# Kernel optimization log

Hardware: AMD Instinct MI355X
Metric: run time of the kernel (lower is better)

The kernel has to match this reference:

```python
import jax, jax.numpy as jnp
import numpy as np

D_MODEL = 256
N_HEADS = 8
N_LEVELS = 4
N_POINTS = 4
DH = D_MODEL // N_HEADS
SHAPES = [(100, 150), (50, 75), (25, 38), (13, 19)]  # per-level (H, W)
BATCH = 2


def setup_inputs() -> dict:
    key = jax.random.key(0)
    ks = jax.random.split(key, 8)
    Lq = sum(h * w for h, w in SHAPES)  # 19947
    d = D_MODEL
    off_dim = N_HEADS * N_LEVELS * N_POINTS * 2
    aw_dim = N_HEADS * N_LEVELS * N_POINTS
    s = 1.0 / np.sqrt(d).astype(np.float32)
    lsi = np.concatenate([[0], np.cumsum([h * w for h, w in SHAPES])[:-1]])
    return {
        "query": jax.random.normal(ks[0], (BATCH, Lq, d), jnp.float32),
        "reference_points": jax.random.uniform(ks[1], (BATCH, Lq, N_LEVELS, 2), jnp.float32),
        "input_flatten": jax.random.normal(ks[2], (BATCH, Lq, d), jnp.float32),
        "input_spatial_shapes": jnp.array(SHAPES, dtype=jnp.int32),
        "input_level_start_index": jnp.array(lsi, dtype=jnp.int32),
        "W_samp": 0.01 * jax.random.normal(ks[3], (off_dim, d), jnp.float32),
        "b_samp": 0.1 * jax.random.normal(ks[4], (off_dim,), jnp.float32),
        "W_attn": s * jax.random.normal(ks[5], (aw_dim, d), jnp.float32),
        "b_attn": jnp.zeros((aw_dim,), jnp.float32),
        "W_val": s * jax.random.normal(ks[6], (d, d), jnp.float32),
        "b_val": jnp.zeros((d,), jnp.float32),
        "W_out": s * jax.random.normal(ks[7], (d, d), jnp.float32),
        "b_out": jnp.zeros((d,), jnp.float32),
    }


def _bilinear(v, grid, Hl, Wl):
    # v: [N, H, Hl*Wl, Dh] flattened level feature map per head
    # grid: [N, H, Q, P, 2] in [-1, 1]; align_corners=False, zero padding
    N, H, Q, P, _ = grid.shape
    Dh = v.shape[-1]
    x = (grid[..., 0] + 1.0) * 0.5 * Wl - 0.5
    y = (grid[..., 1] + 1.0) * 0.5 * Hl - 0.5
    x0 = jnp.floor(x)
    y0 = jnp.floor(y)
    lx = x - x0
    ly = y - y0
    x0i = x0.astype(jnp.int32)
    y0i = y0.astype(jnp.int32)

    def corner(xi, yi, w):
        valid = (xi >= 0) & (xi < Wl) & (yi >= 0) & (yi < Hl)
        idx = jnp.clip(yi, 0, Hl - 1) * Wl + jnp.clip(xi, 0, Wl - 1)
        g = jnp.take_along_axis(v, idx.reshape(N, H, Q * P, 1), axis=2)
        return g.reshape(N, H, Q, P, Dh) * (w * valid)[..., None]

    return (corner(x0i, y0i, (1 - lx) * (1 - ly))
            + corner(x0i + 1, y0i, lx * (1 - ly))
            + corner(x0i, y0i + 1, (1 - lx) * ly)
            + corner(x0i + 1, y0i + 1, lx * ly))


def _forward(query, ref, x, shapes, W_samp, b_samp, W_attn, b_attn, W_val, b_val, W_out, b_out):
    N, Lq, d = query.shape
    H, L, P, Dh = N_HEADS, N_LEVELS, N_POINTS, DH
    # value projection -> [N, H, S, Dh]
    value = (x @ W_val.T + b_val).reshape(N, -1, H, Dh).transpose(0, 2, 1, 3)
    off = (query @ W_samp.T + b_samp).reshape(N, Lq, H, L, P, 2)
    attw = jax.nn.softmax((query @ W_attn.T + b_attn).reshape(N, Lq, H, L * P), axis=-1)
    attw = attw.reshape(N, Lq, H, L, P).transpose(0, 2, 1, 3, 4)  # [N,H,Lq,L,P]
    # offset normalizer is (W, H) per level
    norm = jnp.array([[w, h] for h, w in shapes], dtype=query.dtype)  # [L, 2]
    loc = ref[:, :, None, :, None, :] + off / norm[None, None, None, :, None, :]
    grids = (2.0 * loc - 1.0).transpose(0, 2, 1, 3, 4, 5)  # [N,H,Lq,L,P,2]

    acc = jnp.zeros((N, Lq, H, Dh), query.dtype)
    start = 0
    for lvl, (Hl, Wl) in enumerate(shapes):
        v = value[:, :, start:start + Hl * Wl]  # [N,H,Hl*Wl,Dh]
        start += Hl * Wl
        samp = _bilinear(v, grids[:, :, :, lvl], Hl, Wl)  # [N,H,Lq,P,Dh]
        acc = acc + jnp.einsum('nhqpd,nhqp->nqhd', samp, attw[:, :, :, lvl])
    out = acc.reshape(N, Lq, H * Dh)
    return out @ W_out.T + b_out


def reference(query, reference_points, input_flatten, input_spatial_shapes,
              input_level_start_index, W_samp, b_samp, W_attn, b_attn,
              W_val, b_val, W_out, b_out):
    shapes = [(int(h), int(w)) for h, w in np.asarray(input_spatial_shapes)]
    return _forward(query, reference_points, input_flatten, shapes,
                    W_samp, b_samp, W_attn, b_attn, W_val, b_val, W_out, b_out)
```

## Files before the change

kernel.cpp:

```cpp
#include <hip/hip_runtime.h>
#include <hip/hip_bf16.h>

#define NB 2
#define LQ 19947
#define LV 19947
#define DM 256
#define NH 8
#define NL 4
#define NP 4
#define MROWS (NB*LQ)
#define MPAD  39936
#define QPB 2

__device__ __constant__ int c_lvlH[4] = {100, 50, 25, 13};
__device__ __constant__ int c_lvlW[4] = {150, 75, 38, 19};
__device__ __constant__ int c_lvlS[4] = {0, 15000, 18750, 19700};

typedef __attribute__((ext_vector_type(8))) short short8;
typedef __attribute__((ext_vector_type(4))) float f32x4;

__device__ __forceinline__ unsigned short f2bf(float f) {
  unsigned u = __float_as_uint(f);
  u += 0x7FFFu + ((u >> 16) & 1u);
  return (unsigned short)(u >> 16);
}
__device__ __forceinline__ float bfl(unsigned u) { return __uint_as_float(u << 16); }
__device__ __forceinline__ float bfh(unsigned u) { return __uint_as_float(u & 0xFFFF0000u); }

#define CB_X 9984
__global__ __launch_bounds__(256) void conv_all(
    const float* __restrict__ xin, const float* __restrict__ query,
    const float* __restrict__ Wv, const float* __restrict__ Wsamp,
    const float* __restrict__ Wattn, const float* __restrict__ Wout,
    const float* __restrict__ bsamp, const float* __restrict__ battn,
    unsigned short* __restrict__ xb, unsigned short* __restrict__ qb,
    unsigned short* __restrict__ wvb, unsigned short* __restrict__ wqb,
    unsigned short* __restrict__ wob, float* __restrict__ bsa)
{
  const int b = blockIdx.x, t = threadIdx.x;
  if (b == 2 * CB_X + 224) {
    bsa[t] = bsamp[t];
    if (t < 128) bsa[256 + t] = battn[t];
    return;
  }
  const float* src; unsigned short* dst; int base, ns;
  if (b < CB_X)            { src = xin;   dst = xb;          base = b * 1024;                ns = MROWS * 256; }
  else if (b < 2*CB_X)     { src = query; dst = qb;          base = (b - CB_X) * 1024;       ns = MROWS * 256; }
  else if (b < 2*CB_X+64)  { src = Wv;    dst = wvb;         base = (b - 2*CB_X) * 1024;     ns = 65536; }
  else if (b < 2*CB_X+128) { src = Wsamp; dst = wqb;         base = (b - 2*CB_X-64) * 1024;  ns = 65536; }
  else if (b < 2*CB_X+160) { src = Wattn; dst = wqb + 65536; base = (b - 2*CB_X-128) * 1024; ns = 32768; }
  else                     { src = Wout;  dst = wob;         base = (b - 2*CB_X-160) * 1024; ns = 65536; }
  const int i = base + t * 4;
  ushort4 o;
  if (i + 4 <= ns) {
    const float4 v = *(const float4*)(src + i);
    o.x = f2bf(v.x); o.y = f2bf(v.y); o.z = f2bf(v.z); o.w = f2bf(v.w);
  } else {
    float vs[4];
    #pragma unroll
    for (int j = 0; j < 4; ++j) vs[j] = (i + j < ns) ? src[i + j] : 0.f;
    o.x = f2bf(vs[0]); o.y = f2bf(vs[1]); o.z = f2bf(vs[2]); o.w = f2bf(vs[3]);
  }
  *(ushort4*)(dst + i) = o;
}

__global__ __launch_bounds__(256) void gemm_front(
    const unsigned short* __restrict__ xb, const unsigned short* __restrict__ qb,
    const unsigned short* __restrict__ wvb, const unsigned short* __restrict__ wqb,
    const float* __restrict__ b_val, const float* __restrict__ bsa,
    unsigned short* __restrict__ value, unsigned short* __restrict__ oc)
{
  const unsigned short* Ab; const unsigned short* Wb; const float* bias;
  unsigned short* Cp; int Nn, cb;
  if (blockIdx.y < 2) { Ab = xb; Wb = wvb; bias = b_val; Cp = value; Nn = 256; cb = blockIdx.y; }
  else                { Ab = qb; Wb = wqb; bias = bsa;   Cp = oc;    Nn = 384; cb = blockIdx.y - 2; }

  __shared__ alignas(16) short As[128 * 32];
  __shared__ alignas(16) short Bs[128 * 32];

  const int t = threadIdx.x;
  const int w = t >> 6, l = t & 63;
  const int wr = w >> 1, wc = w & 1;
  const size_t rowBase = (size_t)blockIdx.x * 128;
  const int colBase = cb * 128;

  const f32x4 z = {0.f, 0.f, 0.f, 0.f};
  f32x4 acc[4][4];
  #pragma unroll
  for (int i = 0; i < 4; ++i)
    #pragma unroll
    for (int j = 0; j < 4; ++j) acc[i][j] = z;

  const int srow = l >> 2;
  const int scol = (l & 3) * 8;

  for (int ks = 0; ks < 8; ++ks) {
    const int k0 = ks * 32;
    #pragma unroll
    for (int i = 0; i < 2; ++i) {
      const int ii = w * 2 + i;
      const unsigned short* gA = Ab + (rowBase + ii * 16 + srow) * 256 + k0 + scol;
      __builtin_amdgcn_global_load_lds(
          (const __attribute__((address_space(1))) void*)gA,
          (__attribute__((address_space(3))) void*)&As[ii * 512], 16, 0, 0);
      const unsigned short* gB = Wb + ((size_t)(colBase + ii * 16 + srow)) * 256 + k0 + scol;
      __builtin_amdgcn_global_load_lds(
          (const __attribute__((address_space(1))) void*)gB,
          (__attribute__((address_space(3))) void*)&Bs[ii * 512], 16, 0, 0);
    }
    __syncthreads();
    short8 af[4], bf[4];
    #pragma unroll
    for (int i = 0; i < 4; ++i) {
      af[i] = *(const short8*)&As[(wr * 64 + i * 16 + (l & 15)) * 32 + (l >> 4) * 8];
      bf[i] = *(const short8*)&Bs[(wc * 64 + i * 16 + (l & 15)) * 32 + (l >> 4) * 8];
    }
    #pragma unroll
    for (int i = 0; i < 4; ++i)
      #pragma unroll
      for (int j = 0; j < 4; ++j)
        acc[i][j] = __builtin_amdgcn_mfma_f32_16x16x32_bf16(bf[j], af[i], acc[i][j], 0, 0, 0);
    __syncthreads();
  }

  const int row0 = (int)rowBase + wr * 64 + (l & 15);
  const int col0 = colBase + wc * 64 + (l >> 4) * 4;
  #pragma unroll
  for (int j = 0; j < 4; ++j) {
    const float4 bj = *(const float4*)(bias + col0 + j * 16);
    #pragma unroll
    for (int i = 0; i < 4; ++i) {
      const int row = row0 + i * 16;
      uint2 st;
      st.x = (unsigned)f2bf(acc[i][j][0] + bj.x) | ((unsigned)f2bf(acc[i][j][1] + bj.y) << 16);
      st.y = (unsigned)f2bf(acc[i][j][2] + bj.z) | ((unsigned)f2bf(acc[i][j][3] + bj.w) << 16);
      *(uint2*)(Cp + (size_t)row * Nn + col0 + j * 16) = st;
    }
  }
}

__global__ __launch_bounds__(256) void gemm_out(
    const unsigned short* __restrict__ Ab, const unsigned short* __restrict__ Wb,
    const float* __restrict__ bias, float* __restrict__ Cp)
{
  __shared__ alignas(16) short As[128 * 32];
  __shared__ alignas(16) short Bs[128 * 32];

  const int t = threadIdx.x;
  const int w = t >> 6, l = t & 63;
  const int wr = w >> 1, wc = w & 1;
  const size_t rowBase = (size_t)blockIdx.x * 128;
  const int colBase = blockIdx.y * 128;

  const f32x4 z = {0.f, 0.f, 0.f, 0.f};
  f32x4 acc[4][4];
  #pragma unroll
  for (int i = 0; i < 4; ++i)
    #pragma unroll
    for (int j = 0; j < 4; ++j) acc[i][j] = z;

  const int srow = l >> 2;
  const int scol = (l & 3) * 8;

  for (int ks = 0; ks < 8; ++ks) {
    const int k0 = ks * 32;
    #pragma unroll
    for (int i = 0; i < 2; ++i) {
      const int ii = w * 2 + i;
      const unsigned short* gA = Ab + (rowBase + ii * 16 + srow) * 256 + k0 + scol;
      __builtin_amdgcn_global_load_lds(
          (const __attribute__((address_space(1))) void*)gA,
          (__attribute__((address_space(3))) void*)&As[ii * 512], 16, 0, 0);
      const unsigned short* gB = Wb + ((size_t)(colBase + ii * 16 + srow)) * 256 + k0 + scol;
      __builtin_amdgcn_global_load_lds(
          (const __attribute__((address_space(1))) void*)gB,
          (__attribute__((address_space(3))) void*)&Bs[ii * 512], 16, 0, 0);
    }
    __syncthreads();
    short8 af[4], bf[4];
    #pragma unroll
    for (int i = 0; i < 4; ++i) {
      af[i] = *(const short8*)&As[(wr * 64 + i * 16 + (l & 15)) * 32 + (l >> 4) * 8];
      bf[i] = *(const short8*)&Bs[(wc * 64 + i * 16 + (l & 15)) * 32 + (l >> 4) * 8];
    }
    #pragma unroll
    for (int i = 0; i < 4; ++i)
      #pragma unroll
      for (int j = 0; j < 4; ++j)
        acc[i][j] = __builtin_amdgcn_mfma_f32_16x16x32_bf16(bf[j], af[i], acc[i][j], 0, 0, 0);
    __syncthreads();
  }

  const int row0 = (int)rowBase + wr * 64 + (l & 15);
  const int col0 = colBase + wc * 64 + (l >> 4) * 4;
  #pragma unroll
  for (int j = 0; j < 4; ++j) {
    const float4 bj = *(const float4*)(bias + col0 + j * 16);
    #pragma unroll
    for (int i = 0; i < 4; ++i) {
      const int row = row0 + i * 16;
      if (row < MROWS) {
        *(float4*)(Cp + (size_t)row * 256 + col0 + j * 16) =
            make_float4(acc[i][j][0] + bj.x, acc[i][j][1] + bj.y,
                        acc[i][j][2] + bj.z, acc[i][j][3] + bj.w);
      }
    }
  }
}

__global__ __launch_bounds__(128) void msda_sample(
    const unsigned short* __restrict__ value,
    const float* __restrict__ refp,
    const unsigned short* __restrict__ oc,
    unsigned short* __restrict__ accb)
{
  __shared__ float s_aw[QPB][128];
  __shared__ float s_ref[QPB][8];
  __shared__ alignas(16) unsigned s_poff[QPB][NH][17][4];
  __shared__ alignas(16) float    s_pw[QPB][NH][17][4];

  const int t = threadIdx.x;
  const int bq0 = blockIdx.x * QPB;

  {
    const int q = t >> 6, i = t & 63;
    const int bq = bq0 + q;
    const unsigned pw = *(const unsigned*)(oc + (size_t)bq * 384 + 256 + i * 2);
    s_aw[q][i * 2 + 0] = bfl(pw);
    s_aw[q][i * 2 + 1] = bfh(pw);
    if (t < QPB * 8) {
      const int q2 = t >> 3, j = t & 7;
      s_ref[q2][j] = refp[(size_t)(bq0 + q2) * 8 + j];
    }
  }
  __syncthreads();

  if (t < QPB * NH) {
    const int q = t >> 3, h = t & 7;
    float* aw = &s_aw[q][h * 16];
    float m = aw[0];
    #pragma unroll
    for (int i = 1; i < 16; ++i) m = fmaxf(m, aw[i]);
    float e[16]; float s = 0.f;
    #pragma unroll
    for (int i = 0; i < 16; ++i) { e[i] = __expf(aw[i] - m); s += e[i]; }
    const float inv = 1.f / s;
    #pragma unroll
    for (int i = 0; i < 16; ++i) aw[i] = e[i] * inv;
  }
  __syncthreads();

  #pragma unroll
  for (int it = t; it < QPB * 128; it += 128) {
    const int q = it >> 7, rem = it & 127;
    const int h = rem >> 4, idx = rem & 15;
    const int l = idx >> 2;
    const int bq = bq0 + q;
    const unsigned po = *(const unsigned*)(oc + (size_t)bq * 384 + rem * 2);
    const int Hl = c_lvlH[l], Wl = c_lvlW[l], st = c_lvlS[l];
    const float x = s_ref[q][l * 2 + 0] * (float)Wl - 0.5f + bfl(po);
    const float y = s_ref[q][l * 2 + 1] * (float)Hl - 0.5f + bfh(po);
    const float aw = s_aw[q][rem];
    const float x0f = floorf(x), y0f = floorf(y);
    const float lx = x - x0f, ly = y - y0f;
    const int x0 = (int)x0f, y0 = (int)y0f;
    const float vx0 = (x0 >= 0 && x0 < Wl) ? 1.f : 0.f;
    const float vx1 = (x0 >= -1 && x0 < Wl - 1) ? 1.f : 0.f;
    const float vy0 = (y0 >= 0 && y0 < Hl) ? 1.f : 0.f;
    const float vy1 = (y0 >= -1 && y0 < Hl - 1) ? 1.f : 0.f;
    const int xc0 = min(max(x0, 0), Wl - 1);
    const int xc1 = min(max(x0 + 1, 0), Wl - 1);
    const int yc0 = min(max(y0, 0), Hl - 1);
    const int yc1 = min(max(y0 + 1, 0), Hl - 1);
    const int r0 = st + yc0 * Wl, r1 = st + yc1 * Wl;
    s_poff[q][h][idx][0] = (unsigned)(r0 + xc0) * 512u;
    s_poff[q][h][idx][1] = (unsigned)(r0 + xc1) * 512u;
    s_poff[q][h][idx][2] = (unsigned)(r1 + xc0) * 512u;
    s_poff[q][h][idx][3] = (unsigned)(r1 + xc1) * 512u;
    s_pw[q][h][idx][0] = (1.f - lx) * (1.f - ly) * aw * (vx0 * vy0);
    s_pw[q][h][idx][1] = lx * (1.f - ly) * aw * (vx1 * vy0);
    s_pw[q][h][idx][2] = (1.f - lx) * ly * aw * (vx0 * vy1);
    s_pw[q][h][idx][3] = lx * ly * aw * (vx1 * vy1);
  }
  __syncthreads();

  const int w = t >> 6;
  const int lane = t & 63;
  const int bq = bq0 + w;
  const int n = bq / LQ;
  const char* vbase = (const char*)value + (size_t)n * LV * 512;
  const int h = lane >> 3;
  const int laneoff = h * 64 + (lane & 7) * 8;

  float a0 = 0.f, a1 = 0.f, a2 = 0.f, a3 = 0.f;
  #pragma unroll
  for (int idx = 0; idx < 16; ++idx) {
    const uint4  of = *(const uint4*)&s_poff[w][h][idx][0];
    const float4 wt = *(const float4*)&s_pw[w][h][idx][0];
    const uint2 p00 = *(const uint2*)(vbase + (of.x + laneoff));
    const uint2 p10 = *(const uint2*)(vbase + (of.y + laneoff));
    const uint2 p01 = *(const uint2*)(vbase + (of.z + laneoff));
    const uint2 p11 = *(const uint2*)(vbase + (of.w + laneoff));
    a0 += wt.x * bfl(p00.x) + wt.y * bfl(p10.x) + wt.z * bfl(p01.x) + wt.w * bfl(p11.x);
    a1 += wt.x * bfh(p00.x) + wt.y * bfh(p10.x) + wt.z * bfh(p01.x) + wt.w * bfh(p11.x);
    a2 += wt.x * bfl(p00.y) + wt.y * bfl(p10.y) + wt.z * bfl(p01.y) + wt.w * bfl(p11.y);
    a3 += wt.x * bfh(p00.y) + wt.y * bfh(p10.y) + wt.z * bfh(p01.y) + wt.w * bfh(p11.y);
  }
  ushort4 o;
  o.x = f2bf(a0); o.y = f2bf(a1); o.z = f2bf(a2); o.w = f2bf(a3);
  *(ushort4*)(accb + (size_t)bq * 256 + lane * 4) = o;
}

extern "C" void kernel_launch(void* const* d_in, const int* in_sizes, int n_in,
                              void* d_out, int out_size, void* d_ws, size_t ws_size,
                              hipStream_t stream) {
  const float* query  = (const float*)d_in[0];
  const float* refp   = (const float*)d_in[1];
  const float* xin    = (const float*)d_in[2];
  const float* W_samp = (const float*)d_in[5];
  const float* b_samp = (const float*)d_in[6];
  const float* W_attn = (const float*)d_in[7];
  const float* b_attn = (const float*)d_in[8];
  const float* W_val  = (const float*)d_in[9];
  const float* b_val  = (const float*)d_in[10];
  const float* W_out  = (const float*)d_in[11];
  const float* b_out  = (const float*)d_in[12];
  float* out = (float*)d_out;
  (void)in_sizes; (void)n_in; (void)out_size; (void)ws_size;

  char* ws = (char*)d_ws;
  unsigned short* value = (unsigned short*)(ws);
  unsigned short* qb    = (unsigned short*)(ws + 20447232);
  unsigned short* xb    = (unsigned short*)(ws + 40894464);
  unsigned short* accb  = xb;
  unsigned short* oc    = (unsigned short*)(ws + 61341696);
  unsigned short* wvb   = (unsigned short*)(ws + 92012544);
  unsigned short* wqb   = (unsigned short*)(ws + 92143616);
  unsigned short* wob   = (unsigned short*)(ws + 92340224);
  float*          bsa   = (float*)(ws + 92471296);

  hipLaunchKernelGGL(conv_all, dim3(2 * CB_X + 225), dim3(256), 0, stream,
                     xin, query, W_val, W_samp, W_attn, W_out, b_samp, b_attn,
                     xb, qb, wvb, wqb, wob, bsa);
  hipLaunchKernelGGL(gemm_front, dim3(312, 5), dim3(256), 0, stream,
                     xb, qb, wvb, wqb, b_val, bsa, value, oc);
  hipLaunchKernelGGL(msda_sample, dim3(MROWS / QPB), dim3(128), 0, stream,
                     value, refp, oc, accb);
  hipLaunchKernelGGL(gemm_out, dim3(312, 2), dim3(256), 0, stream,
                     accb, wob, b_out, out);
}
```

Before: 281.5 us.

## Fuse fp32-to-bf16 conversion into GEMM staging and widen sampling loads

Removes the separate conversion kernel. The front and output GEMMs now read fp32 activations and weights directly, converting them to bf16 while staging into LDS, with a row guard for the padded tail. This drops a full read/write pass over the activations and a launch, at the cost of synchronous register-staged loads in place of async global-to-LDS loads and twice the bytes read per GEMM tile. The sampling kernel now handles four queries per block, with 32 lanes per query and 16-byte gathers, plus bounds guards for the ragged final block.

```diff
diff --git a/kernel.cpp b/kernel.cpp
--- a/kernel.cpp
+++ b/kernel.cpp
@@ -10,7 +10,8 @@
 #define NP 4
 #define MROWS (NB*LQ)
 #define MPAD  39936
-#define QPB 2
+#define QPB 4
+#define NOGUARD 0x7FFFFFFF
 
 __device__ __constant__ int c_lvlH[4] = {100, 50, 25, 13};
 __device__ __constant__ int c_lvlW[4] = {150, 75, 38, 19};
@@ -19,62 +20,106 @@
 typedef __attribute__((ext_vector_type(8))) short short8;
 typedef __attribute__((ext_vector_type(4))) float f32x4;
 
-__device__ __forceinline__ unsigned short f2bf(float f) {
-  unsigned u = __float_as_uint(f);
-  u += 0x7FFFu + ((u >> 16) & 1u);
-  return (unsigned short)(u >> 16);
+__device__ __forceinline__ unsigned pk2bf(float x, float y) {
+  __hip_bfloat162 h = __float22bfloat162_rn(make_float2(x, y));
+  unsigned u; __builtin_memcpy(&u, &h, 4); return u;
 }
 __device__ __forceinline__ float bfl(unsigned u) { return __uint_as_float(u << 16); }
 __device__ __forceinline__ float bfh(unsigned u) { return __uint_as_float(u & 0xFFFF0000u); }
 
-#define CB_X 9984
-__global__ __launch_bounds__(256) void conv_all(
+__device__ __forceinline__ void stage_f32(
+    const float* __restrict__ src, int row0, int guard, int k0,
+    short* lds, int t)
+{
+  const int c8 = (t & 3) * 8;
+  #pragma unroll
+  for (int p = 0; p < 2; ++p) {
+    const int r = (t >> 2) + p * 64;
+    const int gr = row0 + r;
+    float4 v0 = make_float4(0.f,0.f,0.f,0.f), v1 = v0;
+    if (gr < guard) {
+      const float* g = src + (size_t)gr * 256 + k0 + c8;
+      v0 = *(const float4*)g;
+      v1 = *(const float4*)(g + 4);
+    }
+    uint4 d;
+    d.x = pk2bf(v0.x, v0.y); d.y = pk2bf(v0.z, v0.w);
+    d.z = pk2bf(v1.x, v1.y); d.w = pk2bf(v1.z, v1.w);
+    *(uint4*)&lds[r * 32 + c8] = d;
+  }
+}
+
+__global__ __launch_bounds__(256) void gemm_front(
     const float* __restrict__ xin, const float* __restrict__ query,
     const float* __restrict__ Wv, const float* __restrict__ Wsamp,
-    const float* __restrict__ Wattn, const float* __restrict__ Wout,
-    const float* __restrict__ bsamp, const float* __restrict__ battn,
-    unsigned short* __restrict__ xb, unsigned short* __restrict__ qb,
-    unsigned short* __restrict__ wvb, unsigned short* __restrict__ wqb,
-    unsigned short* __restrict__ wob, float* __restrict__ bsa)
-{
-  const int b = blockIdx.x, t = threadIdx.x;
-  if (b == 2 * CB_X + 224) {
-    bsa[t] = bsamp[t];
-    if (t < 128) bsa[256 + t] = battn[t];
-    return;
-  }
-  const float* src; unsigned short* dst; int base, ns;
-  if (b < CB_X)            { src = xin;   dst = xb;          base = b * 1024;                ns = MROWS * 256; }
-  else if (b < 2*CB_X)     { src = query; dst = qb;          base = (b - CB_X) * 1024;       ns = MROWS * 256; }
-  else if (b < 2*CB_X+64)  { src = Wv;    dst = wvb;         base = (b - 2*CB_X) * 1024;     ns = 65536; }
-  else if (b < 2*CB_X+128) { src = Wsamp; dst = wqb;         base = (b - 2*CB_X-64) * 1024;  ns = 65536; }
-  else if (b < 2*CB_X+160) { src = Wattn; dst = wqb + 65536; base = (b - 2*CB_X-128) * 1024; ns = 32768; }
-  else                     { src = Wout;  dst = wob;         base = (b - 2*CB_X-160) * 1024; ns = 65536; }
-  const int i = base + t * 4;
-  ushort4 o;
-  if (i + 4 <= ns) {
-    const float4 v = *(const float4*)(src + i);
-    o.x = f2bf(v.x); o.y = f2bf(v.y); o.z = f2bf(v.z); o.w = f2bf(v.w);
-  } else {
-    float vs[4];
-    #pragma unroll
-    for (int j = 0; j < 4; ++j) vs[j] = (i + j < ns) ? src[i + j] : 0.f;
-    o.x = f2bf(vs[0]); o.y = f2bf(vs[1]); o.z = f2bf(vs[2]); o.w = f2bf(vs[3]);
-  }
-  *(ushort4*)(dst + i) = o;
-}
-
-__global__ __launch_bounds__(256) void gemm_front(
-    const unsigned short* __restrict__ xb, const unsigned short* __restrict__ qb,
-    const unsigned short* __restrict__ wvb, const unsigned short* __restrict__ wqb,
-    const float* __restrict__ b_val, const float* __restrict__ bsa,
+    const float* __restrict__ Wattn,
+    const float* __restrict__ b_val, const float* __restrict__ b_samp,
+    const float* __restrict__ b_attn,
     unsigned short* __restrict__ value, unsigned short* __restrict__ oc)
 {
-  const unsigned short* Ab; const unsigned short* Wb; const float* bias;
-  unsigned short* Cp; int Nn, cb;
-  if (blockIdx.y < 2) { Ab = xb; Wb = wvb; bias = b_val; Cp = value; Nn = 256; cb = blockIdx.y; }
-  else                { Ab = qb; Wb = wqb; bias = bsa;   Cp = oc;    Nn = 384; cb = blockIdx.y - 2; }
-
+  const int y = blockIdx.y;
+  const float* Asrc; const float* Bsrc; const float* bias; int bshift;
+  unsigned short* Cp; int Nn, cb, brow0;
+  if (y < 2)      { Asrc = xin;   Bsrc = Wv;    bias = b_val;  bshift = 0;   Cp = value; Nn = 256; cb = y;     brow0 = cb * 128; }
+  else if (y < 4) { Asrc = query; Bsrc = Wsamp; bias = b_samp; bshift = 0;   Cp = oc;    Nn = 384; cb = y - 2; brow0 = cb * 128; }
+  else            { Asrc = query; Bsrc = Wattn; bias = b_attn; bshift = 256; Cp = oc;    Nn = 384; cb = 2;     brow0 = 0; }
+
+  __shared__ alignas(16) short As[128 * 32];
+  __shared__ alignas(16) short Bs[128 * 32];
+
+  const int t = threadIdx.x;
+  const int w = t >> 6, l = t & 63;
+  const int wr = w >> 1, wc = w & 1;
+  const int rowBase = blockIdx.x * 128;
+  const int colBase = cb * 128;
+
+  const f32x4 z = {0.f, 0.f, 0.f, 0.f};
+  f32x4 acc[4][4];
+  #pragma unroll
+  for (int i = 0; i < 4; ++i)
+    #pragma unroll
+    for (int j = 0; j < 4; ++j) acc[i][j] = z;
+
+  for (int ks = 0; ks < 8; ++ks) {
+    const int k0 = ks * 32;
+    stage_f32(Asrc, rowBase, MROWS, k0, As, t);
+    stage_f32(Bsrc, brow0, NOGUARD, k0, Bs, t);
+    __syncthreads();
+    short8 af[4], bf[4];
+    #pragma unroll
+    for (int i = 0; i < 4; ++i) {
+      af[i] = *(const short8*)&As[(wr * 64 + i * 16 + (l & 15)) * 32 + (l >> 4) * 8];
+      bf[i] = *(const short8*)&Bs[(wc * 64 + i * 16 + (l & 15)) * 32 + (l >> 4) * 8];
+    }
+    #pragma unroll
+    for (int i = 0; i < 4; ++i)
+      #pragma unroll
+      for (int j = 0; j < 4; ++j)
+        acc[i][j] = __builtin_amdgcn_mfma_f32_16x16x32_bf16(bf[j], af[i], acc[i][j], 0, 0, 0);
+    __syncthreads();
+  }
+
+  const int row0 = rowBase + wr * 64 + (l & 15);
+  const int col0 = colBase + wc * 64 + (l >> 4) * 4;
+  const float* bb = bias - bshift;
+  #pragma unroll
+  for (int j = 0; j < 4; ++j) {
+    const float4 bj = *(const float4*)(bb + col0 + j * 16);
+    #pragma unroll
+    for (int i = 0; i < 4; ++i) {
+      const int row = row0 + i * 16;
+      uint2 st;
+      st.x = pk2bf(acc[i][j][0] + bj.x, acc[i][j][1] + bj.y);
+      st.y = pk2bf(acc[i][j][2] + bj.z, acc[i][j][3] + bj.w);
+      *(uint2*)(Cp + (size_t)row * Nn + col0 + j * 16) = st;
+    }
+  }
+}
+
+__global__ __launch_bounds__(256) void gemm_out(
+    const unsigned short* __restrict__ Ab, const float* __restrict__ Wsrc,
+    const float* __restrict__ bias, float* __restrict__ Cp)
+{
   __shared__ alignas(16) short As[128 * 32];
   __shared__ alignas(16) short Bs[128 * 32];
 
@@ -82,7 +127,7 @@
   const int w = t >> 6, l = t & 63;
   const int wr = w >> 1, wc = w & 1;
   const size_t rowBase = (size_t)blockIdx.x * 128;
-  const int colBase = cb * 128;
+  const int colBase = blockIdx.y * 128;
 
   const f32x4 z = {0.f, 0.f, 0.f, 0.f};
   f32x4 acc[4][4];
@@ -103,79 +148,8 @@
       __builtin_amdgcn_global_load_lds(
           (const __attribute__((address_space(1))) void*)gA,
           (__attribute__((address_space(3))) void*)&As[ii * 512], 16, 0, 0);
-      const unsigned short* gB = Wb + ((size_t)(colBase + ii * 16 + srow)) * 256 + k0 + scol;
-      __builtin_amdgcn_global_load_lds(
-          (const __attribute__((address_space(1))) void*)gB,
-          (__attribute__((address_space(3))) void*)&Bs[ii * 512], 16, 0, 0);
-    }
-    __syncthreads();
-    short8 af[4], bf[4];
-    #pragma unroll
-    for (int i = 0; i < 4; ++i) {
-      af[i] = *(const short8*)&As[(wr * 64 + i * 16 + (l & 15)) * 32 + (l >> 4) * 8];
-      bf[i] = *(const short8*)&Bs[(wc * 64 + i * 16 + (l & 15)) * 32 + (l >> 4) * 8];
-    }
-    #pragma unroll
-    for (int i = 0; i < 4; ++i)
-      #pragma unroll
-      for (int j = 0; j < 4; ++j)
-        acc[i][j] = __builtin_amdgcn_mfma_f32_16x16x32_bf16(bf[j], af[i], acc[i][j], 0, 0, 0);
-    __syncthreads();
-  }
-
-  const int row0 = (int)rowBase + wr * 64 + (l & 15);
-  const int col0 = colBase + wc * 64 + (l >> 4) * 4;
-  #pragma unroll
-  for (int j = 0; j < 4; ++j) {
-    const float4 bj = *(const float4*)(bias + col0 + j * 16);
-    #pragma unroll
-    for (int i = 0; i < 4; ++i) {
-      const int row = row0 + i * 16;
-      uint2 st;
-      st.x = (unsigned)f2bf(acc[i][j][0] + bj.x) | ((unsigned)f2bf(acc[i][j][1] + bj.y) << 16);
-      st.y = (unsigned)f2bf(acc[i][j][2] + bj.z) | ((unsigned)f2bf(acc[i][j][3] + bj.w) << 16);
-      *(uint2*)(Cp + (size_t)row * Nn + col0 + j * 16) = st;
-    }
-  }
-}
-
-__global__ __launch_bounds__(256) void gemm_out(
-    const unsigned short* __restrict__ Ab, const unsigned short* __restrict__ Wb,
-    const float* __restrict__ bias, float* __restrict__ Cp)
-{
-  __shared__ alignas(16) short As[128 * 32];
-  __shared__ alignas(16) short Bs[128 * 32];
-
-  const int t = threadIdx.x;
-  const int w = t >> 6, l = t & 63;
-  const int wr = w >> 1, wc = w & 1;
-  const size_t rowBase = (size_t)blockIdx.x * 128;
-  const int colBase = blockIdx.y * 128;
-
-  const f32x4 z = {0.f, 0.f, 0.f, 0.f};
-  f32x4 acc[4][4];
-  #pragma unroll
-  for (int i = 0; i < 4; ++i)
-    #pragma unroll
-    for (int j = 0; j < 4; ++j) acc[i][j] = z;
-
-  const int srow = l >> 2;
-  const int scol = (l & 3) * 8;
-
-  for (int ks = 0; ks < 8; ++ks) {
-    const int k0 = ks * 32;
-    #pragma unroll
-    for (int i = 0; i < 2; ++i) {
-      const int ii = w * 2 + i;
-      const unsigned short* gA = Ab + (rowBase + ii * 16 + srow) * 256 + k0 + scol;
-      __builtin_amdgcn_global_load_lds(
-          (const __attribute__((address_space(1))) void*)gA,
-          (__attribute__((address_space(3))) void*)&As[ii * 512], 16, 0, 0);
-      const unsigned short* gB = Wb + ((size_t)(colBase + ii * 16 + srow)) * 256 + k0 + scol;
-      __builtin_amdgcn_global_load_lds(
-          (const __attribute__((address_space(1))) void*)gB,
-          (__attribute__((address_space(3))) void*)&Bs[ii * 512], 16, 0, 0);
-    }
+    }
+    stage_f32(Wsrc, colBase, NOGUARD, k0, Bs, t);
     __syncthreads();
     short8 af[4], bf[4];
     #pragma unroll
@@ -223,30 +197,36 @@
   const int bq0 = blockIdx.x * QPB;
 
   {
-    const int q = t >> 6, i = t & 63;
+    const int q = t >> 5, i = t & 31;
     const int bq = bq0 + q;
-    const unsigned pw = *(const unsigned*)(oc + (size_t)bq * 384 + 256 + i * 2);
-    s_aw[q][i * 2 + 0] = bfl(pw);
-    s_aw[q][i * 2 + 1] = bfh(pw);
+    if (bq < MROWS) {
+      const uint2 pw = *(const uint2*)(oc + (size_t)bq * 384 + 256 + i * 4);
+      s_aw[q][i * 4 + 0] = bfl(pw.x);
+      s_aw[q][i * 4 + 1] = bfh(pw.x);
+      s_aw[q][i * 4 + 2] = bfl(pw.y);
+      s_aw[q][i * 4 + 3] = bfh(pw.y);
+    }
     if (t < QPB * 8) {
       const int q2 = t >> 3, j = t & 7;
-      s_ref[q2][j] = refp[(size_t)(bq0 + q2) * 8 + j];
+      if (bq0 + q2 < MROWS) s_ref[q2][j] = refp[(size_t)(bq0 + q2) * 8 + j];
     }
   }
   __syncthreads();
 
   if (t < QPB * NH) {
     const int q = t >> 3, h = t & 7;
-    float* aw = &s_aw[q][h * 16];
-    float m = aw[0];
-    #pragma unroll
-    for (int i = 1; i < 16; ++i) m = fmaxf(m, aw[i]);
-    float e[16]; float s = 0.f;
-    #pragma unroll
-    for (int i = 0; i < 16; ++i) { e[i] = __expf(aw[i] - m); s += e[i]; }
-    const float inv = 1.f / s;
-    #pragma unroll
-    for (int i = 0; i < 16; ++i) aw[i] = e[i] * inv;
+    if (bq0 + q < MROWS) {
+      float* aw = &s_aw[q][h * 16];
+      float m = aw[0];
+      #pragma unroll
+      for (int i = 1; i < 16; ++i) m = fmaxf(m, aw[i]);
+      float e[16]; float s = 0.f;
+      #pragma unroll
+      for (int i = 0; i < 16; ++i) { e[i] = __expf(aw[i] - m); s += e[i]; }
+      const float inv = 1.f / s;
+      #pragma unroll
+      for (int i = 0; i < 16; ++i) aw[i] = e[i] * inv;
+    }
   }
   __syncthreads();
 
@@ -256,59 +236,67 @@
     const int h = rem >> 4, idx = rem & 15;
     const int l = idx >> 2;
     const int bq = bq0 + q;
-    const unsigned po = *(const unsigned*)(oc + (size_t)bq * 384 + rem * 2);
-    const int Hl = c_lvlH[l], Wl = c_lvlW[l], st = c_lvlS[l];
-    const float x = s_ref[q][l * 2 + 0] * (float)Wl - 0.5f + bfl(po);
-    const float y = s_ref[q][l * 2 + 1] * (float)Hl - 0.5f + bfh(po);
-    const float aw = s_aw[q][rem];
-    const float x0f = floorf(x), y0f = floorf(y);
-    const float lx = x - x0f, ly = y - y0f;
-    const int x0 = (int)x0f, y0 = (int)y0f;
-    const float vx0 = (x0 >= 0 && x0 < Wl) ? 1.f : 0.f;
-    const float vx1 = (x0 >= -1 && x0 < Wl - 1) ? 1.f : 0.f;
-    const float vy0 = (y0 >= 0 && y0 < Hl) ? 1.f : 0.f;
-    const float vy1 = (y0 >= -1 && y0 < Hl - 1) ? 1.f : 0.f;
-    const int xc0 = min(max(x0, 0), Wl - 1);
-    const int xc1 = min(max(x0 + 1, 0), Wl - 1);
-    const int yc0 = min(max(y0, 0), Hl - 1);
-    const int yc1 = min(max(y0 + 1, 0), Hl - 1);
-    const int r0 = st + yc0 * Wl, r1 = st + yc1 * Wl;
-    s_poff[q][h][idx][0] = (unsigned)(r0 + xc0) * 512u;
-    s_poff[q][h][idx][1] = (unsigned)(r0 + xc1) * 512u;
-    s_poff[q][h][idx][2] = (unsigned)(r1 + xc0) * 512u;
-    s_poff[q][h][idx][3] = (unsigned)(r1 + xc1) * 512u;
-    s_pw[q][h][idx][0] = (1.f - lx) * (1.f - ly) * aw * (vx0 * vy0);
-    s_pw[q][h][idx][1] = lx * (1.f - ly) * aw * (vx1 * vy0);
-    s_pw[q][h][idx][2] = (1.f - lx) * ly * aw * (vx0 * vy1);
-    s_pw[q][h][idx][3] = lx * ly * aw * (vx1 * vy1);
+    if (bq < MROWS) {
+      const unsigned po = *(const unsigned*)(oc + (size_t)bq * 384 + rem * 2);
+      const int Hl = c_lvlH[l], Wl = c_lvlW[l], st = c_lvlS[l];
+      const float x = s_ref[q][l * 2 + 0] * (float)Wl - 0.5f + bfl(po);
+      const float y = s_ref[q][l * 2 + 1] * (float)Hl - 0.5f + bfh(po);
+      const float aw = s_aw[q][rem];
+      const float x0f = floorf(x), y0f = floorf(y);
+      const float lx = x - x0f, ly = y - y0f;
+      const int x0 = (int)x0f, y0 = (int)y0f;
+      const float vx0 = (x0 >= 0 && x0 < Wl) ? 1.f : 0.f;
+      const float vx1 = (x0 >= -1 && x0 < Wl - 1) ? 1.f : 0.f;
+      const float vy0 = (y0 >= 0 && y0 < Hl) ? 1.f : 0.f;
+      const float vy1 = (y0 >= -1 && y0 < Hl - 1) ? 1.f : 0.f;
+      const int xc0 = min(max(x0, 0), Wl - 1);
+      const int xc1 = min(max(x0 + 1, 0), Wl - 1);
+      const int yc0 = min(max(y0, 0), Hl - 1);
+      const int yc1 = min(max(y0 + 1, 0), Hl - 1);
+      const int r0 = st + yc0 * Wl, r1 = st + yc1 * Wl;
+      s_poff[q][h][idx][0] = (unsigned)(r0 + xc0) * 512u;
+      s_poff[q][h][idx][1] = (unsigned)(r0 + xc1) * 512u;
+      s_poff[q][h][idx][2] = (unsigned)(r1 + xc0) * 512u;
+      s_poff[q][h][idx][3] = (unsigned)(r1 + xc1) * 512u;
+      s_pw[q][h][idx][0] = (1.f - lx) * (1.f - ly) * aw * (vx0 * vy0);
+      s_pw[q][h][idx][1] = lx * (1.f - ly) * aw * (vx1 * vy0);
+      s_pw[q][h][idx][2] = (1.f - lx) * ly * aw * (vx0 * vy1);
+      s_pw[q][h][idx][3] = lx * ly * aw * (vx1 * vy1);
+    }
   }
   __syncthreads();
 
-  const int w = t >> 6;
-  const int lane = t & 63;
-  const int bq = bq0 + w;
-  const int n = bq / LQ;
-  const char* vbase = (const char*)value + (size_t)n * LV * 512;
-  const int h = lane >> 3;
-  const int laneoff = h * 64 + (lane & 7) * 8;
-
-  float a0 = 0.f, a1 = 0.f, a2 = 0.f, a3 = 0.f;
-  #pragma unroll
-  for (int idx = 0; idx < 16; ++idx) {
-    const uint4  of = *(const uint4*)&s_poff[w][h][idx][0];
-    const float4 wt = *(const float4*)&s_pw[w][h][idx][0];
-    const uint2 p00 = *(const uint2*)(vbase + (of.x + laneoff));
-    const uint2 p10 = *(const uint2*)(vbase + (of.y + laneoff));
-    const uint2 p01 = *(const uint2*)(vbase + (of.z + laneoff));
-    const uint2 p11 = *(const uint2*)(vbase + (of.w + laneoff));
-    a0 += wt.x * bfl(p00.x) + wt.y * bfl(p10.x) + wt.z * bfl(p01.x) + wt.w * bfl(p11.x);
-    a1 += wt.x * bfh(p00.x) + wt.y * bfh(p10.x) + wt.z * bfh(p01.x) + wt.w * bfh(p11.x);
-    a2 += wt.x * bfl(p00.y) + wt.y * bfl(p10.y) + wt.z * bfl(p01.y) + wt.w * bfl(p11.y);
-    a3 += wt.x * bfh(p00.y) + wt.y * bfh(p10.y) + wt.z * bfh(p01.y) + wt.w * bfh(p11.y);
-  }
-  ushort4 o;
-  o.x = f2bf(a0); o.y = f2bf(a1); o.z = f2bf(a2); o.w = f2bf(a3);
-  *(ushort4*)(accb + (size_t)bq * 256 + lane * 4) = o;
+  const int q = t >> 5;
+  const int bq = bq0 + q;
+  const int l32 = t & 31;
+  const int h = l32 >> 2;
+  const int laneoff = h * 64 + (l32 & 3) * 16;
+  if (bq < MROWS) {
+    const int n = bq / LQ;
+    const char* vbase = (const char*)value + (size_t)n * (LV * 512);
+    float a0=0.f,a1=0.f,a2=0.f,a3=0.f,a4=0.f,a5=0.f,a6=0.f,a7=0.f;
+    #pragma unroll
+    for (int idx = 0; idx < 16; ++idx) {
+      const uint4  of = *(const uint4*)&s_poff[q][h][idx][0];
+      const float4 wt = *(const float4*)&s_pw[q][h][idx][0];
+      const uint4 p00 = *(const uint4*)(vbase + (of.x + laneoff));
+      const uint4 p10 = *(const uint4*)(vbase + (of.y + laneoff));
+      const uint4 p01 = *(const uint4*)(vbase + (of.z + laneoff));
+      const uint4 p11 = *(const uint4*)(vbase + (of.w + laneoff));
+      a0 += wt.x*bfl(p00.x) + wt.y*bfl(p10.x) + wt.z*bfl(p01.x) + wt.w*bfl(p11.x);
+      a1 += wt.x*bfh(p00.x) + wt.y*bfh(p10.x) + wt.z*bfh(p01.x) + wt.w*bfh(p11.x);
+      a2 += wt.x*bfl(p00.y) + wt.y*bfl(p10.y) + wt.z*bfl(p01.y) + wt.w*bfl(p11.y);
+      a3 += wt.x*bfh(p00.y) + wt.y*bfh(p10.y) + wt.z*bfh(p01.y) + wt.w*bfh(p11.y);
+      a4 += wt.x*bfl(p00.z) + wt.y*bfl(p10.z) + wt.z*bfl(p01.z) + wt.w*bfl(p11.z);
+      a5 += wt.x*bfh(p00.z) + wt.y*bfh(p10.z) + wt.z*bfh(p01.z) + wt.w*bfh(p11.z);
+      a6 += wt.x*bfl(p00.w) + wt.y*bfl(p10.w) + wt.z*bfl(p01.w) + wt.w*bfl(p11.w);
+      a7 += wt.x*bfh(p00.w) + wt.y*bfh(p10.w) + wt.z*bfh(p01.w) + wt.w*bfh(p11.w);
+    }
+    uint4 o;
+    o.x = pk2bf(a0, a1); o.y = pk2bf(a2, a3);
+    o.z = pk2bf(a4, a5); o.w = pk2bf(a6, a7);
+    *(uint4*)((char*)accb + (size_t)bq * 512 + laneoff) = o;
+  }
 }
 
 extern "C" void kernel_launch(void* const* d_in, const int* in_sizes, int n_in,
@@ -330,22 +318,14 @@
 
   char* ws = (char*)d_ws;
   unsigned short* value = (unsigned short*)(ws);
-  unsigned short* qb    = (unsigned short*)(ws + 20447232);
-  unsigned short* xb    = (unsigned short*)(ws + 40894464);
-  unsigned short* accb  = xb;
-  unsigned short* oc    = (unsigned short*)(ws + 61341696);
-  unsigned short* wvb   = (unsigned short*)(ws + 92012544);
-  unsigned short* wqb   = (unsigned short*)(ws + 92143616);
-  unsigned short* wob   = (unsigned short*)(ws + 92340224);
-  float*          bsa   = (float*)(ws + 92471296);
-
-  hipLaunchKernelGGL(conv_all, dim3(2 * CB_X + 225), dim3(256), 0, stream,
-                     xin, query, W_val, W_samp, W_attn, W_out, b_samp, b_attn,
-                     xb, qb, wvb, wqb, wob, bsa);
+  unsigned short* oc    = (unsigned short*)(ws + 20447232);
+  unsigned short* accb  = (unsigned short*)(ws + 51118080);
+
   hipLaunchKernelGGL(gemm_front, dim3(312, 5), dim3(256), 0, stream,
-                     xb, qb, wvb, wqb, b_val, bsa, value, oc);
-  hipLaunchKernelGGL(msda_sample, dim3(MROWS / QPB), dim3(128), 0, stream,
+                     xin, query, W_val, W_samp, W_attn, b_val, b_samp, b_attn,
+                     value, oc);
+  hipLaunchKernelGGL(msda_sample, dim3((MROWS + QPB - 1) / QPB), dim3(128), 0, stream,
                      value, refp, oc, accb);
   hipLaunchKernelGGL(gemm_out, dim3(312, 2), dim3(256), 0, stream,
-                     accb, wob, b_out, out);
-}
+                     accb, W_out, b_out, out);
+}
```

Result: slower. 299.3 us (+6.3%).

## Keep full-K weight tile resident in LDS and stream A fragments from registers

Applied to the files above, without the earlier changes.

Both GEMM kernels now share a templated routine that loads the whole 128x256 bf16 weight slice into XOR-swizzled shared memory once, then reads A operands directly from global memory into registers with one-step prefetch, with no per-k-step barriers. This removes the repeated LDS staging of A and the two syncs per k-step, and the swizzle is meant to avoid bank conflicts. In exchange it uses 64KB of LDS per block, which lowers occupancy, and A loads bypass LDS sharing, so rows are fetched redundantly by the two column-wave groups.

```diff
diff --git a/kernel.cpp b/kernel.cpp
--- a/kernel.cpp
+++ b/kernel.cpp
@@ -11,6 +11,7 @@
 #define MROWS (NB*LQ)
 #define MPAD  39936
 #define QPB 2
+#define CB_X 9984
 
 __device__ __constant__ int c_lvlH[4] = {100, 50, 25, 13};
 __device__ __constant__ int c_lvlW[4] = {150, 75, 38, 19};
@@ -24,10 +25,12 @@
   u += 0x7FFFu + ((u >> 16) & 1u);
   return (unsigned short)(u >> 16);
 }
+__device__ __forceinline__ unsigned pk2bf(float x, float y) {
+  return (unsigned)f2bf(x) | ((unsigned)f2bf(y) << 16);
+}
 __device__ __forceinline__ float bfl(unsigned u) { return __uint_as_float(u << 16); }
 __device__ __forceinline__ float bfh(unsigned u) { return __uint_as_float(u & 0xFFFF0000u); }
 
-#define CB_X 9984
 __global__ __launch_bounds__(256) void conv_all(
     const float* __restrict__ xin, const float* __restrict__ query,
     const float* __restrict__ Wv, const float* __restrict__ Wsamp,
@@ -64,148 +67,117 @@
   *(ushort4*)(dst + i) = o;
 }
 
+template<int OUT_BF16>
+__device__ __forceinline__ void gemm_bres(
+    unsigned short* Bs,
+    const unsigned short* __restrict__ Ab,
+    const unsigned short* __restrict__ Wb,
+    const float* __restrict__ bias,
+    void* __restrict__ Cp, int Nn, int colBase, int Mstore)
+{
+  const int t = threadIdx.x;
+  const int w = t >> 6, l = t & 63;
+  const int wr = w >> 1, wc = w & 1;
+  const int rowBase = blockIdx.x * 128;
+
+  #pragma unroll
+  for (int r = 0; r < 16; ++r) {
+    const int flat = r * 256 + t;
+    const int col = flat >> 5;
+    const int kc  = flat & 31;
+    const short8 v = *(const short8*)(Wb + (size_t)(colBase + col) * 256 + kc * 8);
+    const int dchunk = col * 32 + (kc ^ (col & 31));
+    *(short8*)&Bs[dchunk * 8] = v;
+  }
+  __syncthreads();
+
+  const f32x4 z = {0.f, 0.f, 0.f, 0.f};
+  f32x4 acc[4][4];
+  #pragma unroll
+  for (int i = 0; i < 4; ++i)
+    #pragma unroll
+    for (int j = 0; j < 4; ++j) acc[i][j] = z;
+
+  const int kb = l >> 4;
+  int arow[4];
+  #pragma unroll
+  for (int i = 0; i < 4; ++i) arow[i] = rowBase + wr * 64 + i * 16 + (l & 15);
+  int bcol[4], bsw[4];
+  #pragma unroll
+  for (int j = 0; j < 4; ++j) {
+    bcol[j] = wc * 64 + j * 16 + (l & 15);
+    bsw[j]  = bcol[j] & 31;
+  }
+
+  short8 a_cur[4], a_nxt[4];
+  #pragma unroll
+  for (int i = 0; i < 4; ++i)
+    a_cur[i] = *(const short8*)(Ab + (size_t)arow[i] * 256 + kb * 8);
+
+  #pragma unroll
+  for (int ks = 0; ks < 8; ++ks) {
+    if (ks < 7) {
+      #pragma unroll
+      for (int i = 0; i < 4; ++i)
+        a_nxt[i] = *(const short8*)(Ab + (size_t)arow[i] * 256 + (ks + 1) * 32 + kb * 8);
+    }
+    short8 bf[4];
+    #pragma unroll
+    for (int j = 0; j < 4; ++j) {
+      const int chunk = bcol[j] * 32 + ((ks * 4 + kb) ^ bsw[j]);
+      bf[j] = *(const short8*)&Bs[chunk * 8];
+    }
+    #pragma unroll
+    for (int i = 0; i < 4; ++i)
+      #pragma unroll
+      for (int j = 0; j < 4; ++j)
+        acc[i][j] = __builtin_amdgcn_mfma_f32_16x16x32_bf16(bf[j], a_cur[i], acc[i][j], 0, 0, 0);
+    #pragma unroll
+    for (int i = 0; i < 4; ++i) a_cur[i] = a_nxt[i];
+  }
+
+  const int row0 = rowBase + wr * 64 + (l & 15);
+  const int col0 = colBase + wc * 64 + (l >> 4) * 4;
+  #pragma unroll
+  for (int j = 0; j < 4; ++j) {
+    const float4 bj = *(const float4*)(bias + col0 + j * 16);
+    #pragma unroll
+    for (int i = 0; i < 4; ++i) {
+      const int row = row0 + i * 16;
+      if (OUT_BF16) {
+        uint2 st;
+        st.x = pk2bf(acc[i][j][0] + bj.x, acc[i][j][1] + bj.y);
+        st.y = pk2bf(acc[i][j][2] + bj.z, acc[i][j][3] + bj.w);
+        *(uint2*)((unsigned short*)Cp + (size_t)row * Nn + col0 + j * 16) = st;
+      } else if (row < Mstore) {
+        *(float4*)((float*)Cp + (size_t)row * Nn + col0 + j * 16) =
+            make_float4(acc[i][j][0] + bj.x, acc[i][j][1] + bj.y,
+                        acc[i][j][2] + bj.z, acc[i][j][3] + bj.w);
+      }
+    }
+  }
+}
+
 __global__ __launch_bounds__(256) void gemm_front(
     const unsigned short* __restrict__ xb, const unsigned short* __restrict__ qb,
     const unsigned short* __restrict__ wvb, const unsigned short* __restrict__ wqb,
     const float* __restrict__ b_val, const float* __restrict__ bsa,
     unsigned short* __restrict__ value, unsigned short* __restrict__ oc)
 {
-  const unsigned short* Ab; const unsigned short* Wb; const float* bias;
-  unsigned short* Cp; int Nn, cb;
-  if (blockIdx.y < 2) { Ab = xb; Wb = wvb; bias = b_val; Cp = value; Nn = 256; cb = blockIdx.y; }
-  else                { Ab = qb; Wb = wqb; bias = bsa;   Cp = oc;    Nn = 384; cb = blockIdx.y - 2; }
-
-  __shared__ alignas(16) short As[128 * 32];
-  __shared__ alignas(16) short Bs[128 * 32];
-
-  const int t = threadIdx.x;
-  const int w = t >> 6, l = t & 63;
-  const int wr = w >> 1, wc = w & 1;
-  const size_t rowBase = (size_t)blockIdx.x * 128;
-  const int colBase = cb * 128;
-
-  const f32x4 z = {0.f, 0.f, 0.f, 0.f};
-  f32x4 acc[4][4];
-  #pragma unroll
-  for (int i = 0; i < 4; ++i)
-    #pragma unroll
-    for (int j = 0; j < 4; ++j) acc[i][j] = z;
-
-  const int srow = l >> 2;
-  const int scol = (l & 3) * 8;
-
-  for (int ks = 0; ks < 8; ++ks) {
-    const int k0 = ks * 32;
-    #pragma unroll
-    for (int i = 0; i < 2; ++i) {
-      const int ii = w * 2 + i;
-      const unsigned short* gA = Ab + (rowBase + ii * 16 + srow) * 256 + k0 + scol;
-      __builtin_amdgcn_global_load_lds(
-          (const __attribute__((address_space(1))) void*)gA,
-          (__attribute__((address_space(3))) void*)&As[ii * 512], 16, 0, 0);
-      const unsigned short* gB = Wb + ((size_t)(colBase + ii * 16 + srow)) * 256 + k0 + scol;
-      __builtin_amdgcn_global_load_lds(
-          (const __attribute__((address_space(1))) void*)gB,
-          (__attribute__((address_space(3))) void*)&Bs[ii * 512], 16, 0, 0);
-    }
-    __syncthreads();
-    short8 af[4], bf[4];
-    #pragma unroll
-    for (int i = 0; i < 4; ++i) {
-      af[i] = *(const short8*)&As[(wr * 64 + i * 16 + (l & 15)) * 32 + (l >> 4) * 8];
-      bf[i] = *(const short8*)&Bs[(wc * 64 + i * 16 + (l & 15)) * 32 + (l >> 4) * 8];
-    }
-    #pragma unroll
-    for (int i = 0; i < 4; ++i)
-      #pragma unroll
-      for (int j = 0; j < 4; ++j)
-        acc[i][j] = __builtin_amdgcn_mfma_f32_16x16x32_bf16(bf[j], af[i], acc[i][j], 0, 0, 0);
-    __syncthreads();
-  }
-
-  const int row0 = (int)rowBase + wr * 64 + (l & 15);
-  const int col0 = colBase + wc * 64 + (l >> 4) * 4;
-  #pragma unroll
-  for (int j = 0; j < 4; ++j) {
-    const float4 bj = *(const float4*)(bias + col0 + j * 16);
-    #pragma unroll
-    for (int i = 0; i < 4; ++i) {
-      const int row = row0 + i * 16;
-      uint2 st;
-      st.x = (unsigned)f2bf(acc[i][j][0] + bj.x) | ((unsigned)f2bf(acc[i][j][1] + bj.y) << 16);
-      st.y = (unsigned)f2bf(acc[i][j][2] + bj.z) | ((unsigned)f2bf(acc[i][j][3] + bj.w) << 16);
-      *(uint2*)(Cp + (size_t)row * Nn + col0 + j * 16) = st;
-    }
-  }
+  __shared__ alignas(16) unsigned short Bs[128 * 256];
+  const int y = blockIdx.y;
+  if (y < 2)
+    gemm_bres<1>(Bs, xb, wvb, b_val, value, 256, y * 128, MPAD);
+  else
+    gemm_bres<1>(Bs, qb, wqb, bsa, oc, 384, (y - 2) * 128, MPAD);
 }
 
 __global__ __launch_bounds__(256) void gemm_out(
-    const unsigned short* __restrict__ Ab, const unsigned short* __restrict__ Wb,
-    const float* __restrict__ bias, float* __restrict__ Cp)
-{
-  __shared__ alignas(16) short As[128 * 32];
-  __shared__ alignas(16) short Bs[128 * 32];
-
-  const int t = threadIdx.x;
-  const int w = t >> 6, l = t & 63;
-  const int wr = w >> 1, wc = w & 1;
-  const size_t rowBase = (size_t)blockIdx.x * 128;
-  const int colBase = blockIdx.y * 128;
-
-  const f32x4 z = {0.f, 0.f, 0.f, 0.f};
-  f32x4 acc[4][4];
-  #pragma unroll
-  for (int i = 0; i < 4; ++i)
-    #pragma unroll
-    for (int j = 0; j < 4; ++j) acc[i][j] = z;
-
-  const int srow = l >> 2;
-  const int scol = (l & 3) * 8;
-
-  for (int ks = 0; ks < 8; ++ks) {
-    const int k0 = ks * 32;
-    #pragma unroll
-    for (int i = 0; i < 2; ++i) {
-      const int ii = w * 2 + i;
-      const unsigned short* gA = Ab + (rowBase + ii * 16 + srow) * 256 + k0 + scol;
-      __builtin_amdgcn_global_load_lds(
-          (const __attribute__((address_space(1))) void*)gA,
-          (__attribute__((address_space(3))) void*)&As[ii * 512], 16, 0, 0);
-      const unsigned short* gB = Wb + ((size_t)(colBase + ii * 16 + srow)) * 256 + k0 + scol;
-      __builtin_amdgcn_global_load_lds(
-          (const __attribute__((address_space(1))) void*)gB,
-          (__attribute__((address_space(3))) void*)&Bs[ii * 512], 16, 0, 0);
-    }
-    __syncthreads();
-    short8 af[4], bf[4];
-    #pragma unroll
-    for (int i = 0; i < 4; ++i) {
-      af[i] = *(const short8*)&As[(wr * 64 + i * 16 + (l & 15)) * 32 + (l >> 4) * 8];
-      bf[i] = *(const short8*)&Bs[(wc * 64 + i * 16 + (l & 15)) * 32 + (l >> 4) * 8];
-    }
-    #pragma unroll
-    for (int i = 0; i < 4; ++i)
-      #pragma unroll
-      for (int j = 0; j < 4; ++j)
-        acc[i][j] = __builtin_amdgcn_mfma_f32_16x16x32_bf16(bf[j], af[i], acc[i][j], 0, 0, 0);
-    __syncthreads();
-  }
-
-  const int row0 = (int)rowBase + wr * 64 + (l & 15);
-  const int col0 = colBase + wc * 64 + (l >> 4) * 4;
-  #pragma unroll
-  for (int j = 0; j < 4; ++j) {
-    const float4 bj = *(const float4*)(bias + col0 + j * 16);
-    #pragma unroll
-    for (int i = 0; i < 4; ++i) {
-      const int row = row0 + i * 16;
-      if (row < MROWS) {
-        *(float4*)(Cp + (size_t)row * 256 + col0 + j * 16) =
-            make_float4(acc[i][j][0] + bj.x, acc[i][j][1] + bj.y,
-                        acc[i][j][2] + bj.z, acc[i][j][3] + bj.w);
-      }
-    }
-  }
+    const unsigned short* __restrict__ accb, const unsigned short* __restrict__ wob,
+    const float* __restrict__ b_out, float* __restrict__ out)
+{
+  __shared__ alignas(16) unsigned short Bs[128 * 256];
+  gemm_bres<0>(Bs, accb, wob, b_out, out, 256, blockIdx.y * 128, MROWS);
 }
 
 __global__ __launch_bounds__(128) void msda_sample(
@@ -288,7 +260,7 @@
   const int lane = t & 63;
   const int bq = bq0 + w;
   const int n = bq / LQ;
-  const char* vbase = (const char*)value + (size_t)n * LV * 512;
+  const char* vbase = (const char*)value + (size_t)n * (LV * 512);
   const int h = lane >> 3;
   const int laneoff = h * 64 + (lane & 7) * 8;
 
```

New measurement: 304.9 us. 8.3% more time.
